# Kernel optimization log

Measured on AMD Instinct MI355X. Metric: run time of the kernel, lower is better.

## Reference

```python
import jax, jax.numpy as jnp
import numpy as np

TAU = 0.5
EPS = 1e-6
RAY_STEPS = 128
N_SECANT = 8
STEPS_IN = 64
STEPS_OUT = 32
RADIUS = 1.0
ADA_START, ADA_END, ADA_DECAY = 2.0, 0.1, 1.5e-5
IT = 100000
DEPTH_NEAR = 0.0
DELTA = float(max(ADA_START * np.exp(-ADA_DECAY * IT), ADA_END))


def _occ_val(p, W1, b1, W2, b2):
    # occupancy probability minus tau (sign change = surface crossing)
    h = jax.nn.softplus(p @ W1 + b1)
    return jax.nn.sigmoid((h @ W2 + b2)[..., 0]) - TAU


def _rgb_alpha(p, v, W1, b1, W2, b2, Wc1, bc1, Wc2, bc2):
    alpha = _occ_val(p, W1, b1, W2, b2) + TAU
    f = jax.nn.relu(jnp.concatenate([p, v], -1) @ Wc1 + bc1)
    rgb = jax.nn.sigmoid(f @ Wc2 + bc2)
    return rgb, alpha


def _forward(pixels, camera_mat, world_mat, scale_mat, W1, b1, W2, b2, Wc1, bc1, Wc2, bc2):
    B, N, _ = pixels.shape
    # transform_to_world with all matrices inverted: p_world = S^-1 W^-1 C^-1 p_hom
    M = jnp.linalg.inv(scale_mat) @ jnp.linalg.inv(world_mat) @ jnp.linalg.inv(camera_mat)
    ones = jnp.ones((B, N, 1), pixels.dtype)
    p_h = jnp.concatenate([pixels, ones, ones], -1)  # (x, y, 1, 1) with depth 1
    pixels_world = jnp.einsum('bij,bnj->bni', M, p_h)[..., :3]
    origin = jnp.array([0.0, 0.0, 0.0, 1.0], pixels.dtype)
    cam0 = jnp.einsum('bij,j->bi', M, origin)[..., :3]                 # (B,3)
    camera_world = jnp.broadcast_to(cam0[:, None, :], (B, N, 3))
    ray = pixels_world - camera_world
    ray = ray / jnp.linalg.norm(ray, axis=-1, keepdims=True)

    # ---- sphere intersection ----
    rcd = jnp.einsum('bnd,bd->bn', ray, cam0)
    under = rcd ** 2 - (jnp.sum(cam0 ** 2, -1)[:, None] - RADIUS ** 2)
    mask_int = under > 0
    s = jnp.sqrt(jnp.where(mask_int, under, 1.0))                      # safe sqrt
    inters = jnp.stack([-s - rcd, s - rcd], -1)
    inters = jnp.where(mask_int[..., None], inters, 0.0)
    inters = jnp.maximum(inters, 0.0)                                  # (B,N,2)
    d_far = inters[..., 1]

    # ---- ray marching + secant root finding (no grad in original) ----
    t = jnp.linspace(0.0, 1.0, RAY_STEPS, dtype=pixels.dtype)
    d_prop = d_far[..., None] * t                                      # (B,N,S)
    p_prop = camera_world[:, :, None, :] + ray[:, :, None, :] * d_prop[..., None]
    val = _occ_val(p_prop, W1, b1, W2, b2)                             # (B,N,S)
    mask_0_free = val[..., 0] < 0
    sign = jnp.sign(val[..., :-1] * val[..., 1:])
    sign = jnp.concatenate([sign, jnp.ones_like(sign[..., :1])], -1)
    cost = sign * jnp.arange(RAY_STEPS, 0, -1, dtype=pixels.dtype)
    ind = jnp.argmin(cost, -1)
    mask_sc = jnp.min(cost, -1) < 0
    f_low = jnp.take_along_axis(val, ind[..., None], -1)[..., 0]
    mask = mask_sc & (f_low < 0) & mask_int & mask_0_free
    ind_hi = jnp.minimum(ind + 1, RAY_STEPS - 1)
    d_low = jnp.take_along_axis(d_prop, ind[..., None], -1)[..., 0]
    d_high = jnp.take_along_axis(d_prop, ind_hi[..., None], -1)[..., 0]
    f_high = jnp.take_along_axis(val, ind_hi[..., None], -1)[..., 0]

    def sec(f_l, f_h, d_l, d_h):
        den = f_h - f_l
        return jnp.where(jnp.abs(den) > 1e-12, -f_l * (d_h - d_l) / den + d_l, 0.5 * (d_l + d_h))

    def body(i, c):
        d_p, d_l, f_l, d_h, f_h = c
        f_m = _occ_val(camera_world + ray * d_p[..., None], W1, b1, W2, b2)
        low = f_m < 0
        d_l = jnp.where(low, d_p, d_l); f_l = jnp.where(low, f_m, f_l)
        d_h = jnp.where(low, d_h, d_p); f_h = jnp.where(low, f_h, f_m)
        return (sec(f_l, f_h, d_l, d_h), d_l, f_l, d_h, f_h)

    d_pred0 = sec(f_low, f_high, d_low, d_high)
    d_pred, _, _, _, _ = jax.lax.fori_loop(0, N_SECANT, body, (d_pred0, d_low, f_low, d_high, f_high))
    d_i = jnp.where(mask, d_pred, jnp.inf)
    d_i = jnp.where(mask_0_free, d_i, 0.0)
    d_i = jax.lax.stop_gradient(d_i)

    # ---- depth interval selection ----
    mask_zero = d_i == 0
    mask_pred = jnp.isfinite(d_i)
    dists = jnp.where(mask_pred, d_i, 1.0)
    dists = jnp.where(mask_zero, 0.0, dists)[0]                        # batch 1, as original
    obj_mask = (mask_pred & ~mask_zero)[0]                             # (N,)
    cam_f = camera_world.reshape(-1, 3)
    ray_f = ray.reshape(-1, 3)
    d_surf = inters.reshape(-1, 2)[:, 1]
    dnp = jnp.maximum(dists - DELTA, DEPTH_NEAR)
    dfp = jnp.minimum(dists + DELTA, d_surf)
    FULL = STEPS_IN + STEPS_OUT
    t_full = jnp.linspace(0.0, 1.0, FULL, dtype=pixels.dtype)
    d_bg = d_surf[:, None] * t_full                                    # depth_range[0] = 0
    t_in = jnp.linspace(0.0, 1.0, STEPS_IN, dtype=pixels.dtype)
    t_out = jnp.linspace(0.0, 1.0, STEPS_OUT, dtype=pixels.dtype)
    d_in = dnp[:, None] * (1.0 - t_in) + dfp[:, None] * t_in
    d_out = dnp[:, None] * t_out
    d_obj = jnp.sort(jnp.concatenate([d_out, d_in], -1), -1)
    d_all = jnp.where(obj_mask[:, None], d_obj, d_bg)                  # (N, FULL)

    # ---- shading + alpha compositing ----
    p_fg = cam_f[:, None, :] + ray_f[:, None, :] * d_all[..., None]    # (N,FULL,3)
    v_fg = jnp.broadcast_to(-ray_f[:, None, :], p_fg.shape)
    rgb, alpha = _rgb_alpha(p_fg, v_fg, W1, b1, W2, b2, Wc1, bc1, Wc2, bc2)
    trans = jnp.cumprod(jnp.concatenate([jnp.ones_like(alpha[:, :1]), 1.0 - alpha + EPS], -1), -1)[:, :-1]
    w = alpha * trans
    rgb_values = jnp.sum(w[..., None] * rgb, -2)
    return rgb_values.reshape(B, N, 3)


def setup_inputs() -> dict:
    key = jax.random.key(0)
    ks = jax.random.split(key, 8)
    B, N, H = 1, 4096, 128
    pixels = jax.random.uniform(ks[0], (B, N, 2), minval=-1.0, maxval=1.0, dtype=jnp.float32)
    camera_mat = jnp.broadcast_to(jnp.diag(jnp.array([2.0, 2.0, 1.0, 1.0], jnp.float32)), (B, 4, 4))
    world_mat = jnp.broadcast_to(jnp.array([[1, 0, 0, 0], [0, 1, 0, 0], [0, 0, 1, 2.0], [0, 0, 0, 1]], jnp.float32), (B, 4, 4))
    scale_mat = jnp.broadcast_to(jnp.eye(4, dtype=jnp.float32), (B, 4, 4))
    W1 = jax.random.normal(ks[1], (3, H), jnp.float32)
    b1 = 0.1 * jax.random.normal(ks[2], (H,), jnp.float32)
    W2 = 0.5 * jax.random.normal(ks[3], (H, 1), jnp.float32)
    b2 = jnp.zeros((1,), jnp.float32)
    Wc1 = 0.5 * jax.random.normal(ks[4], (6, H), jnp.float32)
    bc1 = jnp.zeros((H,), jnp.float32)
    Wc2 = 0.5 * jax.random.normal(ks[5], (H, 3), jnp.float32)
    bc2 = jnp.zeros((3,), jnp.float32)
    return dict(pixels=pixels, camera_mat=camera_mat, world_mat=world_mat, scale_mat=scale_mat,
                W1=W1, b1=b1, W2=W2, b2=b2, Wc1=Wc1, bc1=bc1, Wc2=Wc2, bc2=bc2)


def reference(pixels, camera_mat, world_mat, scale_mat, W1, b1, W2, b2, Wc1, bc1, Wc2, bc2):
    return _forward(pixels, camera_mat, world_mat, scale_mat, W1, b1, W2, b2, Wc1, bc1, Wc2, bc2)
```

## Files before the change

### kernel.cpp

```cpp
#include <hip/hip_runtime.h>
#include <math.h>


namespace {

constexpr int H_    = 128;
constexpr int RS    = 128;
constexpr int NSEC  = 8;
constexpr int SOUT_ = 32;
constexpr int SIN_  = 64;
constexpr int FULL_ = 96;
constexpr float EPSA   = 1e-6f;
constexpr float DELTA_ = 0.44626032029685964f;
constexpr float L2E    = 1.4426950408889634f;
constexpr float LN2    = 0.6931471805599453f;

typedef __attribute__((ext_vector_type(2))) float f2;

__device__ __forceinline__ f2 s2(float v) { return f2{v, v}; }

constexpr float PC0 =  0.5849625007211562f;
constexpr float PC1 =  0.4808983469629878f;
constexpr float PC2 = -0.0801497244938313f;
constexpr float PC3 =  0.0178110498875181f;
constexpr float PC4 = -0.0044527624718795f;
constexpr float PC5 =  0.0011873633258345f;
constexpr float PC6 = -0.0003298231460651f;

__device__ __forceinline__ f2 sp2p(f2 u) {
    f2 e;
    e.x = __builtin_amdgcn_exp2f(-fabsf(u.x));
    e.y = __builtin_amdgcn_exp2f(-fabsf(u.y));
    f2 t = e + e - 1.0f;
    f2 p = s2(PC6);
    p = __builtin_elementwise_fma(p, t, s2(PC5));
    p = __builtin_elementwise_fma(p, t, s2(PC4));
    p = __builtin_elementwise_fma(p, t, s2(PC3));
    p = __builtin_elementwise_fma(p, t, s2(PC2));
    p = __builtin_elementwise_fma(p, t, s2(PC1));
    p = __builtin_elementwise_fma(p, t, s2(PC0));
    return __builtin_elementwise_max(u, s2(0.0f)) + p;
}

__device__ __forceinline__ float sigmoid_fast(float x) {
    return __builtin_amdgcn_rcpf(1.0f + __expf(-x));
}
__device__ __forceinline__ float sgnf(float p) {
    return (p > 0.0f) ? 1.0f : ((p < 0.0f) ? -1.0f : 0.0f);
}
__device__ __forceinline__ float secant_step(float f_l, float f_h, float d_l, float d_h) {
    float den = f_h - f_l;
    if (fabsf(den) > 1e-12f) return -f_l * (d_h - d_l) / den + d_l;
    return 0.5f * (d_l + d_h);
}

__device__ void inv4(const float* m, float* o) {
    float inv[16];
    inv[0]  =  m[5]*m[10]*m[15] - m[5]*m[11]*m[14] - m[9]*m[6]*m[15] + m[9]*m[7]*m[14] + m[13]*m[6]*m[11] - m[13]*m[7]*m[10];
    inv[4]  = -m[4]*m[10]*m[15] + m[4]*m[11]*m[14] + m[8]*m[6]*m[15] - m[8]*m[7]*m[14] - m[12]*m[6]*m[11] + m[12]*m[7]*m[10];
    inv[8]  =  m[4]*m[9]*m[15]  - m[4]*m[11]*m[13] - m[8]*m[5]*m[15] + m[8]*m[7]*m[13] + m[12]*m[5]*m[11] - m[12]*m[7]*m[9];
    inv[12] = -m[4]*m[9]*m[14]  + m[4]*m[10]*m[13] + m[8]*m[5]*m[14] - m[8]*m[6]*m[13] - m[12]*m[5]*m[10] + m[12]*m[6]*m[9];
    inv[1]  = -m[1]*m[10]*m[15] + m[1]*m[11]*m[14] + m[9]*m[2]*m[15] - m[9]*m[3]*m[14] - m[13]*m[2]*m[11] + m[13]*m[3]*m[10];
    inv[5]  =  m[0]*m[10]*m[15] - m[0]*m[11]*m[14] - m[8]*m[2]*m[15] + m[8]*m[3]*m[14] + m[12]*m[2]*m[11] - m[12]*m[3]*m[10];
    inv[9]  = -m[0]*m[9]*m[15]  + m[0]*m[11]*m[13] + m[8]*m[1]*m[15] - m[8]*m[3]*m[13] - m[12]*m[1]*m[11] + m[12]*m[3]*m[9];
    inv[13] =  m[0]*m[9]*m[14]  - m[0]*m[10]*m[13] - m[8]*m[1]*m[14] + m[8]*m[2]*m[13] + m[12]*m[1]*m[10] - m[12]*m[2]*m[9];
    inv[2]  =  m[1]*m[6]*m[15]  - m[1]*m[7]*m[14]  - m[5]*m[2]*m[15] + m[5]*m[3]*m[14] + m[13]*m[2]*m[7]  - m[13]*m[3]*m[6];
    inv[6]  = -m[0]*m[6]*m[15]  + m[0]*m[7]*m[14]  + m[4]*m[2]*m[15] - m[4]*m[3]*m[14] - m[12]*m[2]*m[7]  + m[12]*m[3]*m[6];
    inv[10] =  m[0]*m[5]*m[15]  - m[0]*m[7]*m[13]  - m[4]*m[1]*m[15] + m[4]*m[3]*m[13] + m[12]*m[1]*m[7]  - m[12]*m[3]*m[5];
    inv[14] = -m[0]*m[5]*m[14]  + m[0]*m[6]*m[13]  + m[4]*m[1]*m[14] - m[4]*m[2]*m[13] - m[12]*m[1]*m[6]  + m[12]*m[2]*m[5];
    inv[3]  = -m[1]*m[6]*m[11]  + m[1]*m[7]*m[10]  + m[5]*m[2]*m[11] - m[5]*m[3]*m[10] - m[9]*m[2]*m[7]   + m[9]*m[3]*m[6];
    inv[7]  =  m[0]*m[6]*m[11]  - m[0]*m[7]*m[10]  - m[4]*m[2]*m[11] + m[4]*m[3]*m[10] + m[8]*m[2]*m[7]   - m[8]*m[3]*m[6];
    inv[11] = -m[0]*m[5]*m[11]  + m[0]*m[7]*m[9]   + m[4]*m[1]*m[11] - m[4]*m[3]*m[9]  - m[8]*m[1]*m[7]   + m[8]*m[3]*m[5];
    inv[15] =  m[0]*m[5]*m[10]  - m[0]*m[6]*m[9]   - m[4]*m[1]*m[10] + m[4]*m[2]*m[9]  + m[8]*m[1]*m[6]   - m[8]*m[2]*m[5];
    float det = m[0]*inv[0] + m[1]*inv[4] + m[2]*inv[8] + m[3]*inv[12];
    float idet = 1.0f / det;
    for (int i = 0; i < 16; i++) o[i] = inv[i] * idet;
}

__global__ __launch_bounds__(64) void render_k(
    const float* __restrict__ pixels,
    const float* __restrict__ Cm, const float* __restrict__ Wm, const float* __restrict__ Sm,
    const float* __restrict__ W1, const float* __restrict__ b1,
    const float* __restrict__ W2, const float* __restrict__ b2,
    const float* __restrict__ Wc1, const float* __restrict__ bc1,
    const float* __restrict__ Wc2, const float* __restrict__ bc2,
    float* __restrict__ out, int N)
{
    const int tid = threadIdx.x;
    const int r   = blockIdx.x;

    __shared__ float4 sP0[H_/2];
    __shared__ float4 sP1[H_/2];
    __shared__ float4 sP2[H_/2];
    __shared__ float4 sP3[H_/2];
    __shared__ float  sval[RS];
    __shared__ float  sInv[3][16];
    __shared__ float  sT[16], sM[16];

    {
        const float* mm = (tid == 0) ? Cm : ((tid == 1) ? Wm : Sm);
        float o[16];
        inv4(mm, o);
        if (tid < 3)
            for (int k = 0; k < 16; k++) sInv[tid][k] = o[k];
    }
    __syncthreads();
    if (tid < 16) {
        int row = tid >> 2, col = tid & 3;
        float s = 0.0f;
        for (int k = 0; k < 4; k++) s += sInv[1][row*4 + k] * sInv[0][k*4 + col];
        sT[tid] = s;
    }
    __syncthreads();
    if (tid < 16) {
        int row = tid >> 2, col = tid & 3;
        float s = 0.0f;
        for (int k = 0; k < 4; k++) s += sInv[2][row*4 + k] * sT[k*4 + col];
        sM[tid] = s;
    }
    __syncthreads();

    float cx, cy, cz, rx, ry, rz, dfar;
    int mint;
    {
        const float px_ = pixels[2*r], py_ = pixels[2*r + 1];
        float cam[3], dir[3];
        for (int i = 0; i < 3; i++) {
            cam[i] = sM[4*i + 3];
            float pw = sM[4*i + 0]*px_ + sM[4*i + 1]*py_ + sM[4*i + 2] + sM[4*i + 3];
            dir[i] = pw - cam[i];
        }
        float nrm = sqrtf(dir[0]*dir[0] + dir[1]*dir[1] + dir[2]*dir[2]);
        rx = dir[0]/nrm; ry = dir[1]/nrm; rz = dir[2]/nrm;
        cx = cam[0]; cy = cam[1]; cz = cam[2];
        float rcd = rx*cx + ry*cy + rz*cz;
        float cc  = cx*cx + cy*cy + cz*cz;
        float under = rcd*rcd - (cc - 1.0f);
        mint = under > 0.0f;
        float s = sqrtf(mint ? under : 1.0f);
        dfar = mint ? fmaxf(s - rcd, 0.0f) : 0.0f;
    }

    float a2k[2], c2k[2], w2k[2];
    float cCr[2], w0r[2], w1r[2], w2r[2];
#pragma unroll
    for (int k = 0; k < 2; k++) {
        const int u = 2*tid + k;
        float w1x = W1[u], w1y = W1[H_ + u], w1z = W1[2*H_ + u];
        float b1j = b1[u], w2j = W2[u];
        a2k[k] = (w1x*rx + w1y*ry + w1z*rz) * L2E;
        c2k[k] = (w1x*cx + w1y*cy + w1z*cz + b1j) * L2E;
        w2k[k] = w2j * LN2;
        float q0 = Wc1[u],        q1 = Wc1[H_ + u],  q2 = Wc1[2*H_ + u];
        float q3 = Wc1[3*H_ + u], q4 = Wc1[4*H_ + u], q5 = Wc1[5*H_ + u];
        float aC = q0*rx + q1*ry + q2*rz;
        cCr[k] = q0*cx + q1*cy + q2*cz + bc1[u] - (q3*rx + q4*ry + q5*rz);
        w0r[k] = Wc2[3*u + 0]; w1r[k] = Wc2[3*u + 1]; w2r[k] = Wc2[3*u + 2];
        if (k == 0) {
            sP0[tid].x = a2k[0]; sP0[tid].z = c2k[0];
            sP1[tid].x = w2k[0]; sP1[tid].z = aC;
            sP2[tid].x = cCr[0]; sP2[tid].z = w0r[0];
            sP3[tid].x = w1r[0]; sP3[tid].z = w2r[0];
        } else {
            sP0[tid].y = a2k[1]; sP0[tid].w = c2k[1];
            sP1[tid].y = w2k[1]; sP1[tid].w = aC;
            sP2[tid].y = cCr[1]; sP2[tid].w = w0r[1];
            sP3[tid].y = w1r[1]; sP3[tid].w = w2r[1];
        }
    }
    const float b2v  = b2[0];
    const float bc20 = bc2[0], bc21 = bc2[1], bc22 = bc2[2];
    __syncthreads();

    float alpha0, r0c, g0c, b0c;
    float alpha1, r1c, g1c, b1c;

    if (dfar == 0.0f) {
        f2 sp = sp2p(f2{c2k[0], c2k[1]});
        float part = sp.x*w2k[0] + sp.y*w2k[1];
        f2 ff = __builtin_elementwise_max(f2{cCr[0], cCr[1]}, s2(0.0f));
        float A0 = ff.x*w0r[0] + ff.y*w0r[1];
        float A1 = ff.x*w1r[0] + ff.y*w1r[1];
        float A2 = ff.x*w2r[0] + ff.y*w2r[1];
#pragma unroll
        for (int off = 32; off; off >>= 1) {
            part += __shfl_xor(part, off, 64);
            A0   += __shfl_xor(A0,   off, 64);
            A1   += __shfl_xor(A1,   off, 64);
            A2   += __shfl_xor(A2,   off, 64);
        }
        alpha0 = sigmoid_fast(part + b2v);
        r0c = sigmoid_fast(A0 + bc20);
        g0c = sigmoid_fast(A1 + bc21);
        b0c = sigmoid_fast(A2 + bc22);
        alpha1 = alpha0; r1c = r0c; g1c = g0c; b1c = b0c;
    } else {
        const float inv127 = 1.0f / (RS - 1);
        float l_a, l_b;
        {
            f2 d2 = f2{ dfar * ((float)tid * inv127),
                        dfar * ((float)(tid + 64) * inv127) };
            f2 acc = s2(0.0f);
#pragma unroll 4
            for (int j2 = 0; j2 < H_/2; j2++) {
                float4 q0 = sP0[j2];
                float4 q1 = sP1[j2];
                f2 uA = __builtin_elementwise_fma(s2(q0.x), d2, s2(q0.z));
                f2 uB = __builtin_elementwise_fma(s2(q0.y), d2, s2(q0.w));
                acc = __builtin_elementwise_fma(sp2p(uA), s2(q1.x), acc);
                acc = __builtin_elementwise_fma(sp2p(uB), s2(q1.y), acc);
            }
            l_a = acc.x + b2v;
            l_b = acc.y + b2v;
            sval[tid] = l_a; sval[tid + 64] = l_b;
        }
        __syncthreads();

        float dnp, dfp;
        int obj;
        {
            float va = sigmoid_fast(l_a) - 0.5f;
            float vb = sigmoid_fast(l_b) - 0.5f;
            float van = __shfl_down(va, 1, 64);
            float vb0 = __shfl(vb, 0, 64);
            if (tid == 63) van = vb0;
            float vbn = __shfl_down(vb, 1, 64);
            float ca = sgnf(va * van) * (float)(RS - tid);
            float cb = (tid < 63) ? sgnf(vb * vbn) * (float)(64 - tid) : 1.0f;
            float cmin = ca; int ind = tid;
            if (cb < cmin) { cmin = cb; ind = tid + 64; }
#pragma unroll
            for (int off = 32; off; off >>= 1) {
                float c2 = __shfl_xor(cmin, off, 64);
                int   i2 = __shfl_xor(ind,  off, 64);
                if (c2 < cmin || (c2 == cmin && i2 < ind)) { cmin = c2; ind = i2; }
            }
            const int mask_0_free = (__shfl(va, 0, 64) < 0.0f);
            const int mask_sc = cmin < 0.0f;
            const int ind_hi = min(ind + 1, RS - 1);
            const float f_low  = sigmoid_fast(sval[ind])    - 0.5f;
            const float f_high = sigmoid_fast(sval[ind_hi]) - 0.5f;
            const float d_low  = dfar * ((float)ind    * inv127);
            const float d_high = dfar * ((float)ind_hi * inv127);
            const int msk = mask_sc && (f_low < 0.0f) && mint && mask_0_free;

            float d_p = secant_step(f_low, f_high, d_low, d_high);
            if (msk) {
                float d_l = d_low, f_l = f_low, d_h = d_high, f_h = f_high;
                for (int it = 0; it < NSEC; it++) {
                    f2 u2 = __builtin_elementwise_fma(f2{a2k[0], a2k[1]}, s2(d_p),
                                                      f2{c2k[0], c2k[1]});
                    f2 sp = sp2p(u2);
                    float part = sp.x*w2k[0] + sp.y*w2k[1];
#pragma unroll
                    for (int off = 32; off; off >>= 1) part += __shfl_xor(part, off, 64);
                    float fm = sigmoid_fast(part + b2v) - 0.5f;
                    bool low = fm < 0.0f;
                    d_l = low ? d_p : d_l;  f_l = low ? fm : f_l;
                    d_h = low ? d_h : d_p;  f_h = low ? f_h : fm;
                    d_p = secant_step(f_l, f_h, d_l, d_h);
                }
            }
            float d_i;
            if (!mask_0_free)      d_i = 0.0f;
            else if (msk)          d_i = d_p;
            else                   d_i = INFINITY;
            int mask_zero = (d_i == 0.0f);
            int mask_pred = isfinite(d_i);
            float dists = mask_pred ? d_i : 1.0f;
            if (mask_zero) dists = 0.0f;
            obj = mask_pred && !mask_zero;
            dnp = fmaxf(dists - DELTA_, 0.0f);
            dfp = fminf(dists + DELTA_, dfar);
        }

        auto sample_d = [&](int s) -> float {
            if (obj) {
                if (s < SOUT_) return dnp * ((float)s * (1.0f / (SOUT_ - 1)));
                float u = (float)(s - SOUT_) * (1.0f / (SIN_ - 1));
                return dnp * (1.0f - u) + dfp * u;
            }
            return dfar * ((float)s * (1.0f / (FULL_ - 1)));
        };

        {
            const f2 dd = s2(sample_d(tid));
            f2 SO = s2(0.0f), A0 = s2(0.0f), A1 = s2(0.0f), A2 = s2(0.0f);
#pragma unroll 4
            for (int j2 = 0; j2 < H_/2; j2++) {
                float4 q0 = sP0[j2];
                float4 q1 = sP1[j2];
                float4 q2 = sP2[j2];
                float4 q3 = sP3[j2];
                f2 u = __builtin_elementwise_fma(f2{q0.x, q0.y}, dd, f2{q0.z, q0.w});
                SO = __builtin_elementwise_fma(sp2p(u), f2{q1.x, q1.y}, SO);
                f2 f = __builtin_elementwise_max(
                           __builtin_elementwise_fma(f2{q1.z, q1.w}, dd, f2{q2.x, q2.y}),
                           s2(0.0f));
                A0 = __builtin_elementwise_fma(f, f2{q2.z, q2.w}, A0);
                A1 = __builtin_elementwise_fma(f, f2{q3.x, q3.y}, A1);
                A2 = __builtin_elementwise_fma(f, f2{q3.z, q3.w}, A2);
            }
            alpha0 = sigmoid_fast(SO.x + SO.y + b2v);
            r0c = sigmoid_fast(A0.x + A0.y + bc20);
            g0c = sigmoid_fast(A1.x + A1.y + bc21);
            b0c = sigmoid_fast(A2.x + A2.y + bc22);
        }

        {
            const int s1 = 64 + (tid & 31);
            const int jb = (tid >> 5) * (H_/4);
            const f2 dd = s2(sample_d(s1));
            f2 SO = s2(0.0f), A0 = s2(0.0f), A1 = s2(0.0f), A2 = s2(0.0f);
#pragma unroll 4
            for (int j2 = jb; j2 < jb + H_/4; j2++) {
                float4 q0 = sP0[j2];
                float4 q1 = sP1[j2];
                float4 q2 = sP2[j2];
                float4 q3 = sP3[j2];
                f2 u = __builtin_elementwise_fma(f2{q0.x, q0.y}, dd, f2{q0.z, q0.w});
                SO = __builtin_elementwise_fma(sp2p(u), f2{q1.x, q1.y}, SO);
                f2 f = __builtin_elementwise_max(
                           __builtin_elementwise_fma(f2{q1.z, q1.w}, dd, f2{q2.x, q2.y}),
                           s2(0.0f));
                A0 = __builtin_elementwise_fma(f, f2{q2.z, q2.w}, A0);
                A1 = __builtin_elementwise_fma(f, f2{q3.x, q3.y}, A1);
                A2 = __builtin_elementwise_fma(f, f2{q3.z, q3.w}, A2);
            }
            float SOs = SO.x + SO.y, A0s = A0.x + A0.y;
            float A1s = A1.x + A1.y, A2s = A2.x + A2.y;
            SOs += __shfl_xor(SOs, 32, 64);
            A0s += __shfl_xor(A0s, 32, 64);
            A1s += __shfl_xor(A1s, 32, 64);
            A2s += __shfl_xor(A2s, 32, 64);
            alpha1 = sigmoid_fast(SOs + b2v);
            r1c = sigmoid_fast(A0s + bc20);
            g1c = sigmoid_fast(A1s + bc21);
            b1c = sigmoid_fast(A2s + bc22);
        }
    }

    {
        float mA = 1.0f - alpha0 + EPSA;
        float p = mA;
#pragma unroll
        for (int off = 1; off < 64; off <<= 1) {
            float v = __shfl_up(p, off, 64);
            if (tid >= off) p *= v;
        }
        float TexA = __shfl_up(p, 1, 64);
        if (tid == 0) TexA = 1.0f;
        float TA = __shfl(p, 63, 64);
        float wA = alpha0 * TexA;

        float mB = (tid < 32) ? (1.0f - alpha1 + EPSA) : 1.0f;
        float pb = mB;
#pragma unroll
        for (int off = 1; off < 32; off <<= 1) {
            float v = __shfl_up(pb, off, 64);
            if (tid >= off) pb *= v;
        }
        float TexB = __shfl_up(pb, 1, 64);
        if (tid == 0) TexB = 1.0f;
        float wB = (tid < 32) ? alpha1 * TexB * TA : 0.0f;

        float s0 = wA*r0c + wB*r1c;
        float s1 = wA*g0c + wB*g1c;
        float s2v = wA*b0c + wB*b1c;
#pragma unroll
        for (int off = 32; off; off >>= 1) {
            s0  += __shfl_xor(s0,  off, 64);
            s1  += __shfl_xor(s1,  off, 64);
            s2v += __shfl_xor(s2v, off, 64);
        }
        if (tid == 0) {
            out[3*r + 0] = s0;
            out[3*r + 1] = s1;
            out[3*r + 2] = s2v;
        }
    }
}

}

extern "C" void kernel_launch(void* const* d_in, const int* in_sizes, int n_in,
                              void* d_out, int out_size, void* d_ws, size_t ws_size,
                              hipStream_t stream) {
    const float* pixels = (const float*)d_in[0];
    const float* Cm  = (const float*)d_in[1];
    const float* Wm  = (const float*)d_in[2];
    const float* Sm  = (const float*)d_in[3];
    const float* W1  = (const float*)d_in[4];
    const float* b1  = (const float*)d_in[5];
    const float* W2  = (const float*)d_in[6];
    const float* b2  = (const float*)d_in[7];
    const float* Wc1 = (const float*)d_in[8];
    const float* bc1 = (const float*)d_in[9];
    const float* Wc2 = (const float*)d_in[10];
    const float* bc2 = (const float*)d_in[11];
    float* out = (float*)d_out;

    const int N = in_sizes[0] / 2;
    hipLaunchKernelGGL(render_k, dim3(N), dim3(64), 0, stream,
                       pixels, Cm, Wm, Sm, W1, b1, W2, b2, Wc1, bc1, Wc2, bc2, out, N);
}
```

Measured before the change: 113.9 us.

## Early-exit ray march: evaluate origin first and second half only when needed

The kernel now evaluates the occupancy logit at the ray origin (d=0) first and skips the whole ray march when it is already occupied. Otherwise it marches only the first 64 samples, and evaluates the second 64 only when no sign change is found there, taking crossing values from registers through shuffles instead of shared memory. The inner march loop is also repacked so that each iteration handles two hidden units for one sample, with W2 read from a new shared array. Rays that cross early in the first half save half the MLP evaluations, while rays with no early crossing pay an extra reduction pass and divergent control flow.

New measurement: 98.60 us. -13.4%, faster.

```diff
diff --git a/kernel.cpp b/kernel.cpp
--- a/kernel.cpp
+++ b/kernel.cpp
@@ -93,7 +93,7 @@
     __shared__ float4 sP1[H_/2];
     __shared__ float4 sP2[H_/2];
     __shared__ float4 sP3[H_/2];
-    __shared__ float  sval[RS];
+    __shared__ f2     sW2[H_/2];
     __shared__ float  sInv[3][16];
     __shared__ float  sT[16], sM[16];
 
@@ -168,6 +168,7 @@
             sP3[tid].y = w1r[1]; sP3[tid].w = w2r[1];
         }
     }
+    sW2[tid] = f2{w2k[0], w2k[1]};
     const float b2v  = b2[0];
     const float bc20 = bc2[0], bc21 = bc2[1], bc22 = bc2[2];
     __syncthreads();
@@ -196,57 +197,81 @@
         alpha1 = alpha0; r1c = r0c; g1c = g0c; b1c = b0c;
     } else {
         const float inv127 = 1.0f / (RS - 1);
-        float l_a, l_b;
+
+        float l0;
         {
-            f2 d2 = f2{ dfar * ((float)tid * inv127),
-                        dfar * ((float)(tid + 64) * inv127) };
-            f2 acc = s2(0.0f);
+            f2 sp = sp2p(f2{c2k[0], c2k[1]});
+            float part = sp.x*w2k[0] + sp.y*w2k[1];
+#pragma unroll
+            for (int off = 32; off; off >>= 1) part += __shfl_xor(part, off, 64);
+            l0 = part + b2v;
+        }
+
+        float d_i;
+        if (l0 >= 0.0f) {
+            d_i = 0.0f;
+        } else {
+            auto march_logit = [&](float dsmp) -> float {
+                const f2 dd = s2(dsmp);
+                f2 acc = s2(0.0f);
 #pragma unroll 4
-            for (int j2 = 0; j2 < H_/2; j2++) {
-                float4 q0 = sP0[j2];
-                float4 q1 = sP1[j2];
-                f2 uA = __builtin_elementwise_fma(s2(q0.x), d2, s2(q0.z));
-                f2 uB = __builtin_elementwise_fma(s2(q0.y), d2, s2(q0.w));
-                acc = __builtin_elementwise_fma(sp2p(uA), s2(q1.x), acc);
-                acc = __builtin_elementwise_fma(sp2p(uB), s2(q1.y), acc);
-            }
-            l_a = acc.x + b2v;
-            l_b = acc.y + b2v;
-            sval[tid] = l_a; sval[tid + 64] = l_b;
-        }
-        __syncthreads();
-
-        float dnp, dfp;
-        int obj;
-        {
-            float va = sigmoid_fast(l_a) - 0.5f;
-            float vb = sigmoid_fast(l_b) - 0.5f;
+                for (int j2 = 0; j2 < H_/2; j2++) {
+                    float4 q0 = sP0[j2];
+                    f2 wv = sW2[j2];
+                    f2 u = __builtin_elementwise_fma(f2{q0.x, q0.y}, dd, f2{q0.z, q0.w});
+                    acc = __builtin_elementwise_fma(sp2p(u), wv, acc);
+                }
+                return acc.x + acc.y + b2v;
+            };
+
+            float lA = march_logit(dfar * ((float)tid * inv127));
+            float va = sigmoid_fast(lA) - 0.5f;
             float van = __shfl_down(va, 1, 64);
-            float vb0 = __shfl(vb, 0, 64);
-            if (tid == 63) van = vb0;
-            float vbn = __shfl_down(vb, 1, 64);
-            float ca = sgnf(va * van) * (float)(RS - tid);
-            float cb = (tid < 63) ? sgnf(vb * vbn) * (float)(64 - tid) : 1.0f;
+            float ca = (tid < 63) ? sgnf(va * van) * (float)(RS - tid) : 1.0f;
             float cmin = ca; int ind = tid;
-            if (cb < cmin) { cmin = cb; ind = tid + 64; }
 #pragma unroll
             for (int off = 32; off; off >>= 1) {
                 float c2 = __shfl_xor(cmin, off, 64);
                 int   i2 = __shfl_xor(ind,  off, 64);
                 if (c2 < cmin || (c2 == cmin && i2 < ind)) { cmin = c2; ind = i2; }
             }
-            const int mask_0_free = (__shfl(va, 0, 64) < 0.0f);
-            const int mask_sc = cmin < 0.0f;
-            const int ind_hi = min(ind + 1, RS - 1);
-            const float f_low  = sigmoid_fast(sval[ind])    - 0.5f;
-            const float f_high = sigmoid_fast(sval[ind_hi]) - 0.5f;
-            const float d_low  = dfar * ((float)ind    * inv127);
-            const float d_high = dfar * ((float)ind_hi * inv127);
-            const int msk = mask_sc && (f_low < 0.0f) && mint && mask_0_free;
-
-            float d_p = secant_step(f_low, f_high, d_low, d_high);
+            int crossed = cmin < 0.0f;
+            float f_low = 0.0f, f_high = 0.0f;
+            if (crossed) {
+                f_low  = __shfl(va, ind, 64);
+                f_high = __shfl(va, ind + 1, 64);
+            } else {
+                float lB = march_logit(dfar * ((float)(tid + 64) * inv127));
+                float vb = sigmoid_fast(lB) - 0.5f;
+                float v63 = __shfl(va, 63, 64);
+                float v64 = __shfl(vb, 0, 64);
+                if (v63 * v64 < 0.0f) {
+                    crossed = 1; ind = 63;
+                    f_low = v63; f_high = v64;
+                } else {
+                    float vbn = __shfl_down(vb, 1, 64);
+                    float cb = (tid < 63) ? sgnf(vb * vbn) * (float)(64 - tid) : 1.0f;
+                    float cminb = cb; int indl = tid;
+#pragma unroll
+                    for (int off = 32; off; off >>= 1) {
+                        float c2 = __shfl_xor(cminb, off, 64);
+                        int   i2 = __shfl_xor(indl,  off, 64);
+                        if (c2 < cminb || (c2 == cminb && i2 < indl)) { cminb = c2; indl = i2; }
+                    }
+                    if (cminb < 0.0f) {
+                        crossed = 1; ind = 64 + indl;
+                        f_low  = __shfl(vb, indl, 64);
+                        f_high = __shfl(vb, indl + 1, 64);
+                    }
+                }
+            }
+
+            const int msk = crossed && (f_low < 0.0f) && mint;
             if (msk) {
-                float d_l = d_low, f_l = f_low, d_h = d_high, f_h = f_high;
+                float d_l = dfar * ((float)ind * inv127);
+                float d_h = dfar * ((float)(ind + 1) * inv127);
+                float f_l = f_low, f_h = f_high;
+                float d_p = secant_step(f_l, f_h, d_l, d_h);
                 for (int it = 0; it < NSEC; it++) {
                     f2 u2 = __builtin_elementwise_fma(f2{a2k[0], a2k[1]}, s2(d_p),
                                                       f2{c2k[0], c2k[1]});
@@ -260,19 +285,19 @@
                     d_h = low ? d_h : d_p;  f_h = low ? f_h : fm;
                     d_p = secant_step(f_l, f_h, d_l, d_h);
                 }
-            }
-            float d_i;
-            if (!mask_0_free)      d_i = 0.0f;
-            else if (msk)          d_i = d_p;
-            else                   d_i = INFINITY;
-            int mask_zero = (d_i == 0.0f);
-            int mask_pred = isfinite(d_i);
-            float dists = mask_pred ? d_i : 1.0f;
-            if (mask_zero) dists = 0.0f;
-            obj = mask_pred && !mask_zero;
-            dnp = fmaxf(dists - DELTA_, 0.0f);
-            dfp = fminf(dists + DELTA_, dfar);
-        }
+                d_i = d_p;
+            } else {
+                d_i = INFINITY;
+            }
+        }
+
+        const int mask_zero = (d_i == 0.0f);
+        const int mask_pred = isfinite(d_i);
+        float dists = mask_pred ? d_i : 1.0f;
+        if (mask_zero) dists = 0.0f;
+        const int obj = mask_pred && !mask_zero;
+        const float dnp = fmaxf(dists - DELTA_, 0.0f);
+        const float dfp = fminf(dists + DELTA_, dfar);
 
         auto sample_d = [&](int s) -> float {
             if (obj) {
```
